# Kernel tuning notes

Hardware: AMD Instinct MI355X
Metric: run time of the kernel (lower is better)

The kernel has to match this reference:

```python
import jax, jax.numpy as jnp
import numpy as np

B, N, T, H = 64, 16, 128, 256  # batch, max_neighbors, time_steps, hidden_dim


def setup_inputs() -> dict:
    key = jax.random.key(0)
    ks = jax.random.split(key, 7)
    inv_h = 1.0 / np.sqrt(H)
    return {
        "node_rnn_output": jax.random.normal(ks[0], (B, T, H), jnp.float32),
        "neigh_rnn_output": jax.random.normal(ks[1], (B, N, T, H), jnp.float32),
        "neighbors_number": N,
        "Wq": jax.random.normal(ks[2], (H, H), jnp.float32) * inv_h,
        "Wk": jax.random.normal(ks[3], (H, H), jnp.float32) * inv_h,
        "Wv": jax.random.normal(ks[4], (H, H), jnp.float32) * inv_h,
        "Wb": jax.random.normal(ks[5], (H, H), jnp.float32) * inv_h,
        "b": jnp.zeros((T,), jnp.float32),
    }


def reference(node_rnn_output, neigh_rnn_output, neighbors_number, Wq, Wk, Wv, Wb, b):
    # key_values: node prepended to neighbors -> [B, N+1, T, H]
    kv = jnp.concatenate((node_rnn_output[:, None], neigh_rnn_output), axis=1)
    # torch nn.Linear: x @ W^T
    q = node_rnn_output @ Wq.T            # [B, T, H] (query is identical across neighbor slots)
    key = kv @ Wk.T                       # [B, N+1, T, H]
    value = kv @ Wv.T                     # [B, N+1, T, H]
    # bilinear score: (q @ Wb) @ key^T + b  (b broadcasts over last axis)
    qW = q @ Wb                           # [B, T, H]
    S = jnp.einsum('bth,bnsh->bnts', qW, key) + b  # [B, N+1, T, T]
    A = jax.nn.softmax(S, axis=-1)        # dropout is identity at eval / drop_prob=0
    outputs = jnp.einsum('bnts,bnsh->bnth', A, value)  # [B, N+1, T, H]
    return outputs, A
```

## Files before the change

kernel.cpp:

```cpp
#include <hip/hip_runtime.h>
#include <cstdio>


typedef __bf16 bf16;
typedef __attribute__((ext_vector_type(8))) __bf16 bf16x8;
typedef __attribute__((ext_vector_type(4))) float floatx4;

#define MFMA_BF16 __builtin_amdgcn_mfma_f32_16x16x32_bf16

__device__ __forceinline__ const float* kv_row_ptr(const float* node, const float* neigh, int bn, int s) {
  int b = bn / 17, nn = bn % 17;
  return (nn == 0) ? node + ((size_t)b * 128 + s) * 256
                   : neigh + (((size_t)b * 16 + (nn - 1)) * 128 + s) * 256;
}

__global__ __launch_bounds__(256) void k_wc(const float* __restrict__ Wq, const float* __restrict__ Wb,
                                            float* __restrict__ Wc) {
  int m = blockIdx.x, h = threadIdx.x;
  float acc = 0.f;
  for (int k = 0; k < 256; ++k) acc = fmaf(Wq[k * 256 + m], Wb[k * 256 + h], acc);
  Wc[m * 256 + h] = acc;
}

__global__ __launch_bounds__(256) void k_we(const float* __restrict__ Wc, const float* __restrict__ Wk,
                                            float* __restrict__ We) {
  int m = blockIdx.x, g = threadIdx.x;
  float acc = 0.f;
  for (int k = 0; k < 256; ++k) acc = fmaf(Wc[m * 256 + k], Wk[k * 256 + g], acc);
  We[m * 256 + g] = acc;
}

__global__ __launch_bounds__(256) void k_qwk(const float* __restrict__ X, const float* __restrict__ W,
                                             float* __restrict__ Y) {
  __shared__ float As[32][64];
  __shared__ float Bs[32][64];
  int tid = threadIdx.x;
  int m0 = blockIdx.x * 64, n0 = blockIdx.y * 64;
  int tx = tid & 15, ty = tid >> 4;
  float acc[4][4] = {};
  int r = tid >> 3, c4 = (tid & 7) * 4;
  int kr = tid >> 4, c4b = (tid & 15) * 4;
  for (int k0 = 0; k0 < 256; k0 += 32) {
#pragma unroll
    for (int p = 0; p < 2; ++p) {
      float4 v = *(const float4*)(X + (size_t)(m0 + r + p * 32) * 256 + k0 + c4);
      As[c4 + 0][r + p * 32] = v.x; As[c4 + 1][r + p * 32] = v.y;
      As[c4 + 2][r + p * 32] = v.z; As[c4 + 3][r + p * 32] = v.w;
    }
#pragma unroll
    for (int p = 0; p < 2; ++p) {
      float4 v = *(const float4*)(W + (size_t)(k0 + kr + p * 16) * 256 + n0 + c4b);
      *(float4*)&Bs[kr + p * 16][c4b] = v;
    }
    __syncthreads();
#pragma unroll 8
    for (int k = 0; k < 32; ++k) {
      float a[4], bb[4];
#pragma unroll
      for (int i = 0; i < 4; ++i) a[i] = As[k][ty * 4 + i];
#pragma unroll
      for (int j = 0; j < 4; ++j) bb[j] = Bs[k][tx * 4 + j];
#pragma unroll
      for (int i = 0; i < 4; ++i)
#pragma unroll
        for (int j = 0; j < 4; ++j) acc[i][j] = fmaf(a[i], bb[j], acc[i][j]);
    }
    __syncthreads();
  }
#pragma unroll
  for (int i = 0; i < 4; ++i) {
    float4 v = make_float4(acc[i][0], acc[i][1], acc[i][2], acc[i][3]);
    *(float4*)(Y + (size_t)(m0 + ty * 4 + i) * 256 + n0 + tx * 4) = v;
  }
}

__global__ __launch_bounds__(256) void k_vgemm(const float* __restrict__ node, const float* __restrict__ neigh,
                                               const float* __restrict__ Wv, bf16* __restrict__ V) {
  __shared__ bf16 As[64][32];
  __shared__ bf16 Bs[64][32];
  int tid = threadIdx.x;
  int m0 = blockIdx.x * 64, n0 = blockIdx.y * 64;
  int wave = tid >> 6, lane = tid & 63, lrow = lane & 15, quad = lane >> 4;
  int bn = m0 >> 7, s0 = m0 & 127;
  const float* src = kv_row_ptr(node, neigh, bn, s0);
  floatx4 acc[4];
#pragma unroll
  for (int nt = 0; nt < 4; ++nt) acc[nt] = (floatx4)0.0f;
  int r = tid >> 3, c4 = (tid & 7) * 4;
  for (int k0 = 0; k0 < 256; k0 += 32) {
#pragma unroll
    for (int p = 0; p < 2; ++p) {
      float4 v = *(const float4*)(src + (size_t)(r + p * 32) * 256 + k0 + c4);
      bf16* d = &As[r + p * 32][c4];
      d[0] = (bf16)v.x; d[1] = (bf16)v.y; d[2] = (bf16)v.z; d[3] = (bf16)v.w;
      float4 w = *(const float4*)(Wv + (size_t)(n0 + r + p * 32) * 256 + k0 + c4);
      bf16* d2 = &Bs[r + p * 32][c4];
      d2[0] = (bf16)w.x; d2[1] = (bf16)w.y; d2[2] = (bf16)w.z; d2[3] = (bf16)w.w;
    }
    __syncthreads();
    bf16x8 af = *(const bf16x8*)&As[wave * 16 + lrow][quad * 8];
#pragma unroll
    for (int nt = 0; nt < 4; ++nt) {
      bf16x8 bfv = *(const bf16x8*)&Bs[nt * 16 + lrow][quad * 8];
      acc[nt] = MFMA_BF16(af, bfv, acc[nt], 0, 0, 0);
    }
    __syncthreads();
  }
#pragma unroll
  for (int nt = 0; nt < 4; ++nt)
#pragma unroll
    for (int rg = 0; rg < 4; ++rg)
      V[(size_t)(m0 + wave * 16 + quad * 4 + rg) * 256 + n0 + nt * 16 + lrow] = (bf16)acc[nt][rg];
}

#define QKS 40
#define ABS 136
__global__ __launch_bounds__(256) void k_fused(const float* __restrict__ qWk, const float* __restrict__ node,
                                               const float* __restrict__ neigh, const float* __restrict__ bvec,
                                               const bf16* __restrict__ V,
                                               float* __restrict__ Aout, float* __restrict__ Out) {
  __shared__ __align__(16) char smem[52224];
  bf16* Qhi = (bf16*)smem;
  bf16* Qlo = (bf16*)(smem + 10240);
  bf16* Khi = (bf16*)(smem + 20480);
  bf16* Klo = (bf16*)(smem + 30720);
  bf16* Ab  = (bf16*)smem;
  bf16* Vt  = (bf16*)(smem + 34816);

  int tid = threadIdx.x;
  int w = tid >> 6, lane = tid & 63, lrow = lane & 15, quad = lane >> 4;
  int bn = blockIdx.x;
  const float* Q = qWk + (size_t)(bn / 17) * 128 * 256;
  const float* K = kv_row_ptr(node, neigh, bn, 0);

  int srow = tid >> 1;
  int skb = (tid & 1) * 16;

  floatx4 acc[2][8];
#pragma unroll
  for (int rt = 0; rt < 2; ++rt)
#pragma unroll
    for (int ct = 0; ct < 8; ++ct) acc[rt][ct] = (floatx4)0.0f;

  for (int k0 = 0; k0 < 256; k0 += 32) {
#pragma unroll
    for (int half = 0; half < 2; ++half) {
      const float* qp = Q + (size_t)srow * 256 + k0 + skb + half * 8;
      const float* kp = K + (size_t)srow * 256 + k0 + skb + half * 8;
      float4 q0 = *(const float4*)qp, q1 = *(const float4*)(qp + 4);
      float4 kk0 = *(const float4*)kp, kk1 = *(const float4*)(kp + 4);
      float qf[8] = {q0.x, q0.y, q0.z, q0.w, q1.x, q1.y, q1.z, q1.w};
      float kf[8] = {kk0.x, kk0.y, kk0.z, kk0.w, kk1.x, kk1.y, kk1.z, kk1.w};
      bf16x8 qh, ql, kh, kl;
#pragma unroll
      for (int u = 0; u < 8; ++u) {
        bf16 h = (bf16)qf[u]; qh[u] = h; ql[u] = (bf16)(qf[u] - (float)h);
        bf16 h2 = (bf16)kf[u]; kh[u] = h2; kl[u] = (bf16)(kf[u] - (float)h2);
      }
      int off = srow * QKS + skb + half * 8;
      *(bf16x8*)&Qhi[off] = qh; *(bf16x8*)&Qlo[off] = ql;
      *(bf16x8*)&Khi[off] = kh; *(bf16x8*)&Klo[off] = kl;
    }
    __syncthreads();
    bf16x8 ah[2], al[2];
#pragma unroll
    for (int rt = 0; rt < 2; ++rt) {
      int off = (w * 32 + rt * 16 + lrow) * QKS + quad * 8;
      ah[rt] = *(const bf16x8*)&Qhi[off];
      al[rt] = *(const bf16x8*)&Qlo[off];
    }
#pragma unroll
    for (int ct = 0; ct < 8; ++ct) {
      int off = (ct * 16 + lrow) * QKS + quad * 8;
      bf16x8 bh = *(const bf16x8*)&Khi[off];
      bf16x8 bl = *(const bf16x8*)&Klo[off];
#pragma unroll
      for (int rt = 0; rt < 2; ++rt) {
        acc[rt][ct] = MFMA_BF16(ah[rt], bh, acc[rt][ct], 0, 0, 0);
        acc[rt][ct] = MFMA_BF16(al[rt], bh, acc[rt][ct], 0, 0, 0);
        acc[rt][ct] = MFMA_BF16(ah[rt], bl, acc[rt][ct], 0, 0, 0);
      }
    }
    __syncthreads();
  }

  float bvv[8];
#pragma unroll
  for (int ct = 0; ct < 8; ++ct) bvv[ct] = bvec[ct * 16 + lrow];
#pragma unroll
  for (int rt = 0; rt < 2; ++rt)
#pragma unroll
    for (int r = 0; r < 4; ++r) {
      float mx = -3.402823466e+38f;
#pragma unroll
      for (int ct = 0; ct < 8; ++ct) {
        float v = acc[rt][ct][r] + bvv[ct];
        acc[rt][ct][r] = v;
        mx = fmaxf(mx, v);
      }
#pragma unroll
      for (int off = 1; off < 16; off <<= 1) mx = fmaxf(mx, __shfl_xor(mx, off, 64));
      float s = 0.f;
#pragma unroll
      for (int ct = 0; ct < 8; ++ct) {
        float e = __expf(acc[rt][ct][r] - mx);
        acc[rt][ct][r] = e;
        s += e;
      }
#pragma unroll
      for (int off = 1; off < 16; off <<= 1) s += __shfl_xor(s, off, 64);
      float inv = 1.f / s;
#pragma unroll
      for (int ct = 0; ct < 8; ++ct) acc[rt][ct][r] *= inv;
    }

  float* Ag = Aout + (size_t)bn * 128 * 128;
#pragma unroll
  for (int rt = 0; rt < 2; ++rt)
#pragma unroll
    for (int r = 0; r < 4; ++r) {
      int row = w * 32 + rt * 16 + quad * 4 + r;
#pragma unroll
      for (int ct = 0; ct < 8; ++ct) {
        int s = ct * 16 + lrow;
        float v = acc[rt][ct][r];
        Ag[(size_t)row * 128 + s] = v;
        Ab[row * ABS + s] = (bf16)v;
      }
    }

  const bf16* Vb = V + (size_t)bn * 128 * 256;
  float* Ob = Out + (size_t)bn * 128 * 256;
  int vs = tid & 127, vh = tid >> 7;
  for (int h0 = 0; h0 < 256; h0 += 64) {
#pragma unroll
    for (int it = 0; it < 4; ++it) {
      int idx8 = it * 2 + vh;
      bf16x8 v = *(const bf16x8*)&Vb[(size_t)vs * 256 + h0 + idx8 * 8];
#pragma unroll
      for (int u = 0; u < 8; ++u) Vt[(idx8 * 8 + u) * ABS + vs] = v[u];
    }
    __syncthreads();
    floatx4 pacc[2][4];
#pragma unroll
    for (int rt = 0; rt < 2; ++rt)
#pragma unroll
      for (int ct = 0; ct < 4; ++ct) pacc[rt][ct] = (floatx4)0.0f;
#pragma unroll
    for (int s0 = 0; s0 < 128; s0 += 32) {
      bf16x8 af[2];
#pragma unroll
      for (int rt = 0; rt < 2; ++rt)
        af[rt] = *(const bf16x8*)&Ab[(w * 32 + rt * 16 + lrow) * ABS + s0 + quad * 8];
#pragma unroll
      for (int ct = 0; ct < 4; ++ct) {
        bf16x8 bv8 = *(const bf16x8*)&Vt[(ct * 16 + lrow) * ABS + s0 + quad * 8];
#pragma unroll
        for (int rt = 0; rt < 2; ++rt)
          pacc[rt][ct] = MFMA_BF16(af[rt], bv8, pacc[rt][ct], 0, 0, 0);
      }
    }
#pragma unroll
    for (int rt = 0; rt < 2; ++rt)
#pragma unroll
      for (int ct = 0; ct < 4; ++ct)
#pragma unroll
        for (int r = 0; r < 4; ++r) {
          int row = w * 32 + rt * 16 + quad * 4 + r;
          Ob[(size_t)row * 256 + h0 + ct * 16 + lrow] = pacc[rt][ct][r];
        }
    __syncthreads();
  }
}

extern "C" void kernel_launch(void* const* d_in, const int* in_sizes, int n_in,
                              void* d_out, int out_size, void* d_ws, size_t ws_size,
                              hipStream_t stream) {
  const float* node  = (const float*)d_in[0];
  const float* neigh = (const float*)d_in[1];
  const float* Wq = (const float*)d_in[3];
  const float* Wk = (const float*)d_in[4];
  const float* Wv = (const float*)d_in[5];
  const float* Wb = (const float*)d_in[6];
  const float* bv = (const float*)d_in[7];

  float* out  = (float*)d_out;
  float* Aout = out + (size_t)64 * 17 * 128 * 256;

  size_t need = (size_t)(65536 + 65536 + 2097152) * 4 + (size_t)35651584 * 2;
  if (ws_size < need) { fprintf(stderr, "ws too small: %zu < %zu\n", ws_size, need); return; }
  float* wsf = (float*)d_ws;
  float* Wc  = wsf;
  float* We  = wsf + 65536;
  float* qWk = wsf + 131072;
  bf16*  V   = (bf16*)(wsf + 131072 + 2097152);

  k_wc<<<256, 256, 0, stream>>>(Wq, Wb, Wc);
  k_we<<<256, 256, 0, stream>>>(Wc, Wk, We);
  k_qwk<<<dim3(128, 4), 256, 0, stream>>>(node, We, qWk);
  k_vgemm<<<dim3(2176, 4), 256, 0, stream>>>(node, neigh, Wv, V);
  k_fused<<<1088, 256, 0, stream>>>(qWk, node, neigh, bv, V, Aout, out);
}
```

Before: 526.5 us.

## Fuse V projection into attention kernel, drop separate V GEMM and buffer

Removes the standalone V projection kernel and its ~71MB bf16 intermediate. Each fused block now recomputes its own V tile from the kv rows and a pre-converted bf16 Wv, chunked by 64 hidden columns, and writes it transposed into shared memory for the A·V MFMA. This trades a global write and re-read of V for rereading K rows from global four times (once per h0 chunk) and extra in-block MFMA work and barriers.

```diff
diff --git a/kernel.cpp b/kernel.cpp
--- a/kernel.cpp
+++ b/kernel.cpp
@@ -4,6 +4,7 @@
 
 typedef __bf16 bf16;
 typedef __attribute__((ext_vector_type(8))) __bf16 bf16x8;
+typedef __attribute__((ext_vector_type(4))) __bf16 bf16x4;
 typedef __attribute__((ext_vector_type(4))) float floatx4;
 
 #define MFMA_BF16 __builtin_amdgcn_mfma_f32_16x16x32_bf16
@@ -28,6 +29,14 @@
   float acc = 0.f;
   for (int k = 0; k < 256; ++k) acc = fmaf(Wc[m * 256 + k], Wk[k * 256 + g], acc);
   We[m * 256 + g] = acc;
+}
+
+__global__ __launch_bounds__(256) void k_wvb(const float* __restrict__ Wv, bf16* __restrict__ Wvb) {
+  int i = (blockIdx.x * 256 + threadIdx.x) * 4;
+  float4 v = *(const float4*)(Wv + i);
+  bf16x4 o;
+  o[0] = (bf16)v.x; o[1] = (bf16)v.y; o[2] = (bf16)v.z; o[3] = (bf16)v.w;
+  *(bf16x4*)(Wvb + i) = o;
 }
 
 __global__ __launch_bounds__(256) void k_qwk(const float* __restrict__ X, const float* __restrict__ W,
@@ -74,50 +83,12 @@
   }
 }
 
-__global__ __launch_bounds__(256) void k_vgemm(const float* __restrict__ node, const float* __restrict__ neigh,
-                                               const float* __restrict__ Wv, bf16* __restrict__ V) {
-  __shared__ bf16 As[64][32];
-  __shared__ bf16 Bs[64][32];
-  int tid = threadIdx.x;
-  int m0 = blockIdx.x * 64, n0 = blockIdx.y * 64;
-  int wave = tid >> 6, lane = tid & 63, lrow = lane & 15, quad = lane >> 4;
-  int bn = m0 >> 7, s0 = m0 & 127;
-  const float* src = kv_row_ptr(node, neigh, bn, s0);
-  floatx4 acc[4];
-#pragma unroll
-  for (int nt = 0; nt < 4; ++nt) acc[nt] = (floatx4)0.0f;
-  int r = tid >> 3, c4 = (tid & 7) * 4;
-  for (int k0 = 0; k0 < 256; k0 += 32) {
-#pragma unroll
-    for (int p = 0; p < 2; ++p) {
-      float4 v = *(const float4*)(src + (size_t)(r + p * 32) * 256 + k0 + c4);
-      bf16* d = &As[r + p * 32][c4];
-      d[0] = (bf16)v.x; d[1] = (bf16)v.y; d[2] = (bf16)v.z; d[3] = (bf16)v.w;
-      float4 w = *(const float4*)(Wv + (size_t)(n0 + r + p * 32) * 256 + k0 + c4);
-      bf16* d2 = &Bs[r + p * 32][c4];
-      d2[0] = (bf16)w.x; d2[1] = (bf16)w.y; d2[2] = (bf16)w.z; d2[3] = (bf16)w.w;
-    }
-    __syncthreads();
-    bf16x8 af = *(const bf16x8*)&As[wave * 16 + lrow][quad * 8];
-#pragma unroll
-    for (int nt = 0; nt < 4; ++nt) {
-      bf16x8 bfv = *(const bf16x8*)&Bs[nt * 16 + lrow][quad * 8];
-      acc[nt] = MFMA_BF16(af, bfv, acc[nt], 0, 0, 0);
-    }
-    __syncthreads();
-  }
-#pragma unroll
-  for (int nt = 0; nt < 4; ++nt)
-#pragma unroll
-    for (int rg = 0; rg < 4; ++rg)
-      V[(size_t)(m0 + wave * 16 + quad * 4 + rg) * 256 + n0 + nt * 16 + lrow] = (bf16)acc[nt][rg];
-}
-
 #define QKS 40
 #define ABS 136
+#define KVS 68
 __global__ __launch_bounds__(256) void k_fused(const float* __restrict__ qWk, const float* __restrict__ node,
                                                const float* __restrict__ neigh, const float* __restrict__ bvec,
-                                               const bf16* __restrict__ V,
+                                               const bf16* __restrict__ Wvb,
                                                float* __restrict__ Aout, float* __restrict__ Out) {
   __shared__ __align__(16) char smem[52224];
   bf16* Qhi = (bf16*)smem;
@@ -125,6 +96,7 @@
   bf16* Khi = (bf16*)(smem + 20480);
   bf16* Klo = (bf16*)(smem + 30720);
   bf16* Ab  = (bf16*)smem;
+  bf16* Kvb = (bf16*)(smem + 34816);
   bf16* Vt  = (bf16*)(smem + 34816);
 
   int tid = threadIdx.x;
@@ -229,18 +201,60 @@
       }
     }
 
-  const bf16* Vb = V + (size_t)bn * 128 * 256;
   float* Ob = Out + (size_t)bn * 128 * 256;
-  int vs = tid & 127, vh = tid >> 7;
+  int vrow = tid >> 1, vkb = (tid & 1) * 32;
   for (int h0 = 0; h0 < 256; h0 += 64) {
-#pragma unroll
-    for (int it = 0; it < 4; ++it) {
-      int idx8 = it * 2 + vh;
-      bf16x8 v = *(const bf16x8*)&Vb[(size_t)vs * 256 + h0 + idx8 * 8];
-#pragma unroll
-      for (int u = 0; u < 8; ++u) Vt[(idx8 * 8 + u) * ABS + vs] = v[u];
-    }
-    __syncthreads();
+    floatx4 vacc[2][4];
+#pragma unroll
+    for (int rt = 0; rt < 2; ++rt)
+#pragma unroll
+      for (int ct = 0; ct < 4; ++ct) vacc[rt][ct] = (floatx4)0.0f;
+
+    for (int k0 = 0; k0 < 256; k0 += 64) {
+      bf16x8 bwv[2][4];
+#pragma unroll
+      for (int ks = 0; ks < 2; ++ks)
+#pragma unroll
+        for (int ct = 0; ct < 4; ++ct)
+          bwv[ks][ct] = *(const bf16x8*)&Wvb[(size_t)(h0 + ct * 16 + lrow) * 256 + k0 + ks * 32 + quad * 8];
+      {
+        const float* kp = K + (size_t)vrow * 256 + k0 + vkb;
+        bf16* d = &Kvb[vrow * KVS + vkb];
+#pragma unroll
+        for (int j = 0; j < 4; ++j) {
+          float4 a = *(const float4*)(kp + j * 8);
+          float4 b2 = *(const float4*)(kp + j * 8 + 4);
+          bf16x8 o;
+          o[0] = (bf16)a.x;  o[1] = (bf16)a.y;  o[2] = (bf16)a.z;  o[3] = (bf16)a.w;
+          o[4] = (bf16)b2.x; o[5] = (bf16)b2.y; o[6] = (bf16)b2.z; o[7] = (bf16)b2.w;
+          *(bf16x8*)(d + j * 8) = o;
+        }
+      }
+      __syncthreads();
+#pragma unroll
+      for (int ks = 0; ks < 2; ++ks) {
+        bf16x8 af[2];
+#pragma unroll
+        for (int rt = 0; rt < 2; ++rt)
+          af[rt] = *(const bf16x8*)&Kvb[(w * 32 + rt * 16 + lrow) * KVS + ks * 32 + quad * 8];
+#pragma unroll
+        for (int ct = 0; ct < 4; ++ct)
+#pragma unroll
+          for (int rt = 0; rt < 2; ++rt)
+            vacc[rt][ct] = MFMA_BF16(af[rt], bwv[ks][ct], vacc[rt][ct], 0, 0, 0);
+      }
+      __syncthreads();
+    }
+
+#pragma unroll
+    for (int ct = 0; ct < 4; ++ct)
+#pragma unroll
+      for (int rt = 0; rt < 2; ++rt)
+#pragma unroll
+        for (int r = 0; r < 4; ++r)
+          Vt[(ct * 16 + lrow) * ABS + w * 32 + rt * 16 + quad * 4 + r] = (bf16)vacc[rt][ct][r];
+    __syncthreads();
+
     floatx4 pacc[2][4];
 #pragma unroll
     for (int rt = 0; rt < 2; ++rt)
@@ -287,17 +301,17 @@
   float* out  = (float*)d_out;
   float* Aout = out + (size_t)64 * 17 * 128 * 256;
 
-  size_t need = (size_t)(65536 + 65536 + 2097152) * 4 + (size_t)35651584 * 2;
+  size_t need = (size_t)(65536 + 65536 + 2097152) * 4 + (size_t)65536 * 2;
   if (ws_size < need) { fprintf(stderr, "ws too small: %zu < %zu\n", ws_size, need); return; }
   float* wsf = (float*)d_ws;
   float* Wc  = wsf;
   float* We  = wsf + 65536;
   float* qWk = wsf + 131072;
-  bf16*  V   = (bf16*)(wsf + 131072 + 2097152);
-
+  bf16*  Wvb = (bf16*)(wsf + 131072 + 2097152);
+
+  k_wvb<<<64, 256, 0, stream>>>(Wv, Wvb);
   k_wc<<<256, 256, 0, stream>>>(Wq, Wb, Wc);
   k_we<<<256, 256, 0, stream>>>(Wc, Wk, We);
   k_qwk<<<dim3(128, 4), 256, 0, stream>>>(node, We, qWk);
-  k_vgemm<<<dim3(2176, 4), 256, 0, stream>>>(node, neigh, Wv, V);
-  k_fused<<<1088, 256, 0, stream>>>(qWk, node, neigh, bv, V, Aout, out);
-}
+  k_fused<<<1088, 256, 0, stream>>>(qWk, node, neigh, bv, Wvb, Aout, out);
+}
```

Measured after the change: 548.9 us. 1.04x slower.
